# Kernel optimization log

Hardware: AMD Instinct MI355X
Metric: run time of the kernel (lower is better)

The kernel has to match this reference:

```python
import jax, jax.numpy as jnp
import numpy as np

K = 3  # knn interpolation neighbors (init kwarg k)
EPS = 1e-8


def _knn_interpolate(x, pos, pos_skip, B, k):
    # Uniform per-batch counts (guaranteed by setup_inputs) let us vectorize the
    # per-batch cdist+topk+gather chain as batched dense ops.
    Nc = pos.shape[0] // B
    Nf = pos_skip.shape[0] // B
    C = x.shape[1]
    pc = pos.reshape(B, Nc, 3)        # coarse positions
    pf = pos_skip.reshape(B, Nf, 3)   # fine (target) positions
    xc = x.reshape(B, Nc, C)          # coarse features
    # squared pairwise distances via gemm: [B, Nf, Nc]
    d2 = (jnp.sum(pf * pf, -1)[:, :, None]
          + jnp.sum(pc * pc, -1)[:, None, :]
          - 2.0 * jnp.einsum('bfd,bcd->bfc', pf, pc))
    _, idx = jax.lax.top_k(-d2, k)    # k nearest coarse indices per fine point
    b = jnp.arange(B)[:, None, None]
    nb_pos = pc[b, idx]                              # [B,Nf,k,3]
    diff = nb_pos - pf[:, :, None, :]
    dist = jnp.sqrt(jnp.sum(diff * diff, -1))        # exact same dist math as torch
    w = 1.0 / (dist + EPS)                           # [B,Nf,k]
    feats = xc[b, idx]                               # [B,Nf,k,C]
    num = jnp.einsum('bfkc,bfk->bfc', feats, w)
    den = jnp.sum(w, -1, keepdims=True) + EPS
    return (num / den).reshape(B * Nf, C)


def setup_inputs() -> dict:
    key = jax.random.key(0)
    ks = jax.random.split(key, 6)
    B, Nc, Nf, C, Cs, H = 16, 1024, 4096, 512, 256, 512
    x = jax.random.normal(ks[0], (B * Nc, C), jnp.float32)
    pos = jax.random.normal(ks[1], (B * Nc, 3), jnp.float32)
    batch = jnp.repeat(jnp.arange(B, dtype=jnp.int64), Nc)
    x_skip = jax.random.normal(ks[2], (B * Nf, Cs), jnp.float32)
    pos_skip = jax.random.normal(ks[3], (B * Nf, 3), jnp.float32)
    batch_skip = jnp.repeat(jnp.arange(B, dtype=jnp.int64), Nf)
    # MLP params (self.nn = MLP 768 -> 512 -> 512, ReLU)
    W1 = jax.random.normal(ks[4], (C + Cs, H), jnp.float32) / np.sqrt(C + Cs).astype(np.float32)
    b1 = jnp.zeros((H,), jnp.float32)
    W2 = jax.random.normal(ks[5], (H, H), jnp.float32) / np.sqrt(H).astype(np.float32)
    b2 = jnp.zeros((H,), jnp.float32)
    return dict(x=x, pos=pos, batch=batch, x_skip=x_skip, pos_skip=pos_skip,
                batch_skip=batch_skip, W1=W1, b1=b1, W2=W2, b2=b2)


def reference(x, pos, batch, x_skip, pos_skip, batch_skip, W1, b1, W2, b2):
    B = int(np.asarray(batch).max()) + 1
    h = _knn_interpolate(x, pos, pos_skip, B, K)   # [N_fine, C]
    h = jnp.concatenate([h, x_skip], axis=1)       # skip connection concat
    h = jax.nn.relu(h @ W1 + b1)
    h = jax.nn.relu(h @ W2 + b2)
    return h
```

## Files before the change

kernel.cpp:

```cpp
#include <hip/hip_runtime.h>
#include <stdint.h>

typedef __attribute__((ext_vector_type(8))) short short8;
typedef __attribute__((ext_vector_type(4))) float f32x4;

static __device__ __forceinline__ ushort f2bf(float f) {
  uint32_t u = __float_as_uint(f);
  uint32_t r = (u + 0x7FFFu + ((u >> 16) & 1u)) >> 16;
  return (ushort)r;
}
static __device__ __forceinline__ float bf2f(ushort h) {
  return __uint_as_float(((uint32_t)h) << 16);
}

static __device__ __forceinline__ void ins3b(double d, int i,
    double& b0, double& b1, double& b2, int& i0, int& i1, int& i2) {
  const bool c0 = d < b0, c1 = d < b1, c2 = d < b2;
  const double nb0 = c0 ? d : b0;
  const int    ni0 = c0 ? i : i0;
  const double nb1 = c0 ? b0 : (c1 ? d : b1);
  const int    ni1 = c0 ? i0 : (c1 ? i : i1);
  const double nb2 = c1 ? b1 : (c2 ? d : b2);
  const int    ni2 = c1 ? i1 : (c2 ? i : i2);
  b0 = nb0; b1 = nb1; b2 = nb2; i0 = ni0; i1 = ni1; i2 = ni2;
}

__global__ __launch_bounds__(256) void prep_kernel(
    const float* __restrict__ pos, const float* __restrict__ pos_skip,
    const float* __restrict__ x, const float* __restrict__ xs,
    const float* __restrict__ W1, const float* __restrict__ W2,
    int4* __restrict__ idx_out, float4* __restrict__ w_out,
    ushort* __restrict__ xbf, ushort* __restrict__ xsbf,
    ushort* __restrict__ W1at, ushort* __restrict__ W1bt,
    ushort* __restrict__ W2t)
{
  __shared__ float pc4[4096];
  if (blockIdx.x < 1024) {
    const int b   = blockIdx.x >> 6;
    const int blk = blockIdx.x & 63;
    for (int i = threadIdx.x; i < 1024; i += 256) {
      const float* ps = pos + (size_t)b * 3072 + i * 3;
      float4 v = { ps[0], ps[1], ps[2], 0.f };
      *(float4*)&pc4[i * 4] = v;
    }
    __syncthreads();

    const int p   = threadIdx.x >> 2;
    const int sub = threadIdx.x & 3;
    const int row = b * 4096 + blk * 64 + p;
    const float pxf = pos_skip[(size_t)row * 3 + 0];
    const float pyf = pos_skip[(size_t)row * 3 + 1];
    const float pzf = pos_skip[(size_t)row * 3 + 2];

    uint32_t c0 = 0xFFFFFFFFu, c1 = 0xFFFFFFFFu, c2 = 0xFFFFFFFFu, c3 = 0xFFFFFFFFu;
    auto ins4u = [&](uint32_t k) {
      const bool l0 = k < c0, l1 = k < c1, l2 = k < c2, l3 = k < c3;
      const uint32_t n0 = l0 ? k  : c0;
      const uint32_t n1 = l0 ? c0 : (l1 ? k : c1);
      const uint32_t n2 = l1 ? c1 : (l2 ? k : c2);
      const uint32_t n3 = l2 ? c2 : (l3 ? k : c3);
      c0 = n0; c1 = n1; c2 = n2; c3 = n3;
    };
#pragma unroll 4
    for (int j = 0; j < 256; ++j) {
      const int i = j * 4 + sub;
      const float4 q = *(const float4*)&pc4[i * 4];
      const float dx = q.x - pxf;
      const float dy = q.y - pyf;
      const float dz = q.z - pzf;
      const float d = fmaf(dx, dx, fmaf(dy, dy, dz * dz));
      ins4u((__float_as_uint(d) & 0xFFFFFC00u) | (uint32_t)i);
    }
#pragma unroll
    for (int m = 1; m <= 2; m <<= 1) {
      const uint32_t e0 = (uint32_t)__shfl_xor((int)c0, m);
      const uint32_t e1 = (uint32_t)__shfl_xor((int)c1, m);
      const uint32_t e2 = (uint32_t)__shfl_xor((int)c2, m);
      const uint32_t e3 = (uint32_t)__shfl_xor((int)c3, m);
      ins4u(e0); ins4u(e1); ins4u(e2); ins4u(e3);
    }
    if (sub == 0) {
      const double pxd = (double)pxf, pyd = (double)pyf, pzd = (double)pzf;
      auto exd = [&](int i) -> double {
        const double dx = (double)pc4[i * 4 + 0] - pxd;
        const double dy = (double)pc4[i * 4 + 1] - pyd;
        const double dz = (double)pc4[i * 4 + 2] - pzd;
        return dx * dx + dy * dy + dz * dz;
      };
      const int j0 = (int)(c0 & 1023u), j1 = (int)(c1 & 1023u);
      const int j2 = (int)(c2 & 1023u), j3 = (int)(c3 & 1023u);
      double b0 = 1e300, b1 = 1e300, b2 = 1e300;
      int i0 = 0, i1 = 0, i2 = 0;
      ins3b(exd(j0), j0, b0, b1, b2, i0, i1, i2);
      ins3b(exd(j1), j1, b0, b1, b2, i0, i1, i2);
      ins3b(exd(j2), j2, b0, b1, b2, i0, i1, i2);
      ins3b(exd(j3), j3, b0, b1, b2, i0, i1, i2);
      const double w0 = 1.0 / (sqrt(b0) + 1e-8);
      const double w1 = 1.0 / (sqrt(b1) + 1e-8);
      const double w2 = 1.0 / (sqrt(b2) + 1e-8);
      const double den = w0 + w1 + w2 + 1e-8;
      idx_out[row] = make_int4(i0, i1, i2, 0);
      w_out[row] = make_float4((float)(w0 / den), (float)(w1 / den), (float)(w2 / den), 0.f);
    }
  } else if (blockIdx.x < 3072) {
    const int id = (blockIdx.x - 1024) * 256 + threadIdx.x;
#pragma unroll
    for (int it = 0; it < 4; ++it) {
      const int i = id + it * 524288;
      const float4 v = *(const float4*)(x + (size_t)i * 4);
      ushort4 o = { f2bf(v.x), f2bf(v.y), f2bf(v.z), f2bf(v.w) };
      *(ushort4*)(xbf + (size_t)i * 4) = o;
    }
  } else if (blockIdx.x < 7168) {
    const int id = (blockIdx.x - 3072) * 256 + threadIdx.x;
#pragma unroll
    for (int it = 0; it < 4; ++it) {
      const int i = id + it * 1048576;
      const float4 v = *(const float4*)(xs + (size_t)i * 4);
      ushort4 o = { f2bf(v.x), f2bf(v.y), f2bf(v.z), f2bf(v.w) };
      *(ushort4*)(xsbf + (size_t)i * 4) = o;
    }
  } else {
    const int id = (blockIdx.x - 7168) * 256 + threadIdx.x;
    if (id < 262144) {
      const int n = id >> 9, k = id & 511;
      W1at[id] = f2bf(W1[(size_t)k * 512 + n]);
    } else if (id < 393216) {
      const int id2 = id - 262144;
      const int n = id2 >> 8, k = id2 & 255;
      W1bt[id2] = f2bf(W1[(size_t)(512 + k) * 512 + n]);
    } else if (id < 655360) {
      const int id3 = id - 393216;
      const int n = id3 >> 9, k = id3 & 511;
      W2t[id3] = f2bf(W2[(size_t)k * 512 + n]);
    }
  }
}

template<int K, bool OUT_BF16, bool ACT>
__global__ __launch_bounds__(512, 2) void gemm_bias_relu(
    const ushort* __restrict__ A, const ushort* __restrict__ Bt,
    const float* __restrict__ bias, void* __restrict__ Cout, int M, int N)
{
  constexpr int BM = 256, BN = 256, BK = 64, NT = K / BK;
  __shared__ ushort Asm[2][BM * BK];
  __shared__ ushort Bsm[2][BN * BK];
  const int tid  = threadIdx.x;
  const int lane = tid & 63;
  const int wave = tid >> 6;

  const int cpx  = gridDim.x >> 3;
  const int wgid = (blockIdx.x & 7) * cpx + (blockIdx.x >> 3);
  const int nbn  = N / BN;
  const int bm   = wgid / nbn;
  const int bn   = wgid - bm * nbn;
  const int row0 = bm * BM, col0 = bn * BN;
  const int wr = wave >> 2, wc = wave & 3;
  const int sbase = wave * 4096 + lane * 16;

  f32x4 acc[8][4] = {};

  auto stageA = [&](int buf, int kt) {
#pragma unroll
    for (int i = 0; i < 4; ++i) {
      const int o = sbase + i * 1024;
      const int r = o >> 7, s = (o & 127) >> 4;
      __builtin_amdgcn_global_load_lds(
          (const __attribute__((address_space(1))) void*)(A + (size_t)(row0 + r) * K + kt * BK + ((s ^ (r & 7)) << 3)),
          (__attribute__((address_space(3))) void*)((char*)&Asm[buf][0] + o), 16, 0, 0);
    }
  };
  auto stageB = [&](int buf, int kt) {
#pragma unroll
    for (int i = 0; i < 4; ++i) {
      const int o = sbase + i * 1024;
      const int r = o >> 7, s = (o & 127) >> 4;
      __builtin_amdgcn_global_load_lds(
          (const __attribute__((address_space(1))) void*)(Bt + (size_t)(col0 + r) * K + kt * BK + ((s ^ (r & 7)) << 3)),
          (__attribute__((address_space(3))) void*)((char*)&Bsm[buf][0] + o), 16, 0, 0);
    }
  };
  auto rdA = [&](int buf, int mi, int kk) -> short8 {
    const int ra = wr * 128 + mi * 16 + (lane & 15);
    const int s  = kk * 4 + (lane >> 4);
    return *(const short8*)((const char*)&Asm[buf][0] + ra * 128 + ((s ^ (ra & 7)) << 4));
  };
  auto rdB = [&](int buf, int ni, int kk) -> short8 {
    const int rb = wc * 64 + ni * 16 + (lane & 15);
    const int s  = kk * 4 + (lane >> 4);
    return *(const short8*)((const char*)&Bsm[buf][0] + rb * 128 + ((s ^ (rb & 7)) << 4));
  };

  stageA(0, 0); stageB(0, 0);
  asm volatile("s_waitcnt vmcnt(0)" ::: "memory");
  __builtin_amdgcn_s_barrier();

  int cur = 0;
#pragma unroll 1
  for (int t = 0; t < NT; ++t) {
    short8 av[4], bv[4];
#pragma unroll
    for (int mi = 0; mi < 4; ++mi) av[mi] = rdA(cur, mi, 0);
#pragma unroll
    for (int ni = 0; ni < 4; ++ni) bv[ni] = rdB(cur, ni, 0);
    if (t + 1 < NT) stageA(cur ^ 1, t + 1);
    __builtin_amdgcn_s_barrier();
    asm volatile("s_waitcnt lgkmcnt(0)" ::: "memory");
    __builtin_amdgcn_sched_barrier(0);
    __builtin_amdgcn_s_setprio(1);
#pragma unroll
    for (int mi = 0; mi < 4; ++mi)
#pragma unroll
      for (int ni = 0; ni < 4; ++ni)
        acc[mi][ni] = __builtin_amdgcn_mfma_f32_16x16x32_bf16(av[mi], bv[ni], acc[mi][ni], 0, 0, 0);
    __builtin_amdgcn_s_setprio(0);
    __builtin_amdgcn_s_barrier();
#pragma unroll
    for (int mi = 0; mi < 4; ++mi) av[mi] = rdA(cur, 4 + mi, 0);
    if (t + 1 < NT) stageB(cur ^ 1, t + 1);
    __builtin_amdgcn_s_barrier();
    asm volatile("s_waitcnt lgkmcnt(0)" ::: "memory");
    __builtin_amdgcn_sched_barrier(0);
    __builtin_amdgcn_s_setprio(1);
#pragma unroll
    for (int mi = 0; mi < 4; ++mi)
#pragma unroll
      for (int ni = 0; ni < 4; ++ni)
        acc[4 + mi][ni] = __builtin_amdgcn_mfma_f32_16x16x32_bf16(av[mi], bv[ni], acc[4 + mi][ni], 0, 0, 0);
    __builtin_amdgcn_s_setprio(0);
    __builtin_amdgcn_s_barrier();
#pragma unroll
    for (int mi = 0; mi < 4; ++mi) av[mi] = rdA(cur, mi, 1);
#pragma unroll
    for (int ni = 0; ni < 4; ++ni) bv[ni] = rdB(cur, ni, 1);
    __builtin_amdgcn_s_barrier();
    asm volatile("s_waitcnt lgkmcnt(0)" ::: "memory");
    __builtin_amdgcn_sched_barrier(0);
    __builtin_amdgcn_s_setprio(1);
#pragma unroll
    for (int mi = 0; mi < 4; ++mi)
#pragma unroll
      for (int ni = 0; ni < 4; ++ni)
        acc[mi][ni] = __builtin_amdgcn_mfma_f32_16x16x32_bf16(av[mi], bv[ni], acc[mi][ni], 0, 0, 0);
    __builtin_amdgcn_s_setprio(0);
    __builtin_amdgcn_s_barrier();
#pragma unroll
    for (int mi = 0; mi < 4; ++mi) av[mi] = rdA(cur, 4 + mi, 1);
    __builtin_amdgcn_s_barrier();
    asm volatile("s_waitcnt lgkmcnt(0)" ::: "memory");
    __builtin_amdgcn_sched_barrier(0);
    __builtin_amdgcn_s_setprio(1);
#pragma unroll
    for (int mi = 0; mi < 4; ++mi)
#pragma unroll
      for (int ni = 0; ni < 4; ++ni)
        acc[4 + mi][ni] = __builtin_amdgcn_mfma_f32_16x16x32_bf16(av[mi], bv[ni], acc[4 + mi][ni], 0, 0, 0);
    __builtin_amdgcn_s_setprio(0);
    asm volatile("s_waitcnt vmcnt(0)" ::: "memory");
    __builtin_amdgcn_s_barrier();
    cur ^= 1;
  }

  const int lc = lane & 15, lr = lane >> 4;
#pragma unroll
  for (int mi = 0; mi < 8; ++mi) {
#pragma unroll
    for (int ni = 0; ni < 4; ++ni) {
      const int col = col0 + wc * 64 + ni * 16 + lc;
      float bv2 = 0.f;
      if constexpr (ACT) bv2 = bias[col];
      const int rbase = row0 + wr * 128 + mi * 16 + lr * 4;
#pragma unroll
      for (int r = 0; r < 4; ++r) {
        float v = acc[mi][ni][r];
        if constexpr (ACT) { v += bv2; v = v > 0.f ? v : 0.f; }
        if (OUT_BF16) ((ushort*)Cout)[(size_t)(rbase + r) * N + col] = f2bf(v);
        else          ((float*)Cout)[(size_t)(rbase + r) * N + col] = v;
      }
    }
  }
}

__global__ __launch_bounds__(256, 2) void gemm128_combine(
    const ushort* __restrict__ A, const ushort* __restrict__ Bt,
    const float* __restrict__ bias, ushort* __restrict__ h2,
    const ushort* __restrict__ Ybf, const int4* __restrict__ idx3,
    const float4* __restrict__ w3)
{
  constexpr int K = 256, N = 512, BM = 128, BN = 128, BK = 64, NT = K / BK;
  __shared__ ushort Asm[2][BM * BK];
  __shared__ ushort Bsm[2][BN * BK];
  const int tid  = threadIdx.x;
  const int lane = tid & 63;
  const int wave = tid >> 6;

  const int cpx  = gridDim.x >> 3;
  const int wgid = (blockIdx.x & 7) * cpx + (blockIdx.x >> 3);
  const int nbn  = N / BN;
  const int bm   = wgid / nbn;
  const int bn   = wgid - bm * nbn;
  const int row0 = bm * BM, col0 = bn * BN;
  const int wr = wave >> 1, wc = wave & 1;
  const int so = tid * 16;

  f32x4 acc[4][4] = {};

  auto stage = [&](int buf, int kt) {
#pragma unroll
    for (int i = 0; i < 4; ++i) {
      const int o = i * 4096 + so;
      const int r = o >> 7, s = (o & 127) >> 4;
      const int cu = ((s ^ (r & 7)) << 3);
      __builtin_amdgcn_global_load_lds(
          (const __attribute__((address_space(1))) void*)(A + (size_t)(row0 + r) * K + kt * BK + cu),
          (__attribute__((address_space(3))) void*)((char*)&Asm[buf][0] + o), 16, 0, 0);
      __builtin_amdgcn_global_load_lds(
          (const __attribute__((address_space(1))) void*)(Bt + (size_t)(col0 + r) * K + kt * BK + cu),
          (__attribute__((address_space(3))) void*)((char*)&Bsm[buf][0] + o), 16, 0, 0);
    }
  };
  auto compute = [&](int buf) {
#pragma unroll
    for (int kk = 0; kk < 2; ++kk) {
      short8 af[4], bfr[4];
#pragma unroll
      for (int mi = 0; mi < 4; ++mi) {
        const int ra = wr * 64 + mi * 16 + (lane & 15);
        const int s  = kk * 4 + (lane >> 4);
        af[mi] = *(const short8*)&Asm[buf][ra * BK + ((s ^ (ra & 7)) << 3)];
      }
#pragma unroll
      for (int ni = 0; ni < 4; ++ni) {
        const int rb = wc * 64 + ni * 16 + (lane & 15);
        const int s  = kk * 4 + (lane >> 4);
        bfr[ni] = *(const short8*)&Bsm[buf][rb * BK + ((s ^ (rb & 7)) << 3)];
      }
#pragma unroll
      for (int mi = 0; mi < 4; ++mi)
#pragma unroll
        for (int ni = 0; ni < 4; ++ni)
          acc[mi][ni] = __builtin_amdgcn_mfma_f32_16x16x32_bf16(af[mi], bfr[ni], acc[mi][ni], 0, 0, 0);
    }
  };

  stage(0, 0);
  __syncthreads();
  int cur = 0;
#pragma unroll 1
  for (int kt = 0; kt < NT - 1; ++kt) {
    stage(cur ^ 1, kt + 1);
    compute(cur);
    __syncthreads();
    cur ^= 1;
  }
  compute(cur);

  const int lc = lane & 15, lr = lane >> 4;
#pragma unroll
  for (int mi = 0; mi < 4; ++mi) {
#pragma unroll
    for (int r = 0; r < 4; ++r) {
      const int row = row0 + wr * 64 + mi * 16 + lr * 4 + r;
      const int4 id = idx3[row];
      const float4 w = w3[row];
      const ushort* Yb = Ybf + (size_t)(row >> 12) * 524288;
      const ushort* y0 = Yb + (size_t)id.x * 512;
      const ushort* y1 = Yb + (size_t)id.y * 512;
      const ushort* y2 = Yb + (size_t)id.z * 512;
#pragma unroll
      for (int ni = 0; ni < 4; ++ni) {
        const int col = col0 + wc * 64 + ni * 16 + lc;
        float v = acc[mi][ni][r]
                + w.x * bf2f(y0[col])
                + w.y * bf2f(y1[col])
                + w.z * bf2f(y2[col])
                + bias[col];
        v = v > 0.f ? v : 0.f;
        h2[(size_t)row * 512 + col] = f2bf(v);
      }
    }
  }
}

extern "C" void kernel_launch(void* const* d_in, const int* in_sizes, int n_in,
                              void* d_out, int out_size, void* d_ws, size_t ws_size,
                              hipStream_t stream) {
  const float* x        = (const float*)d_in[0];
  const float* pos      = (const float*)d_in[1];
  const float* x_skip   = (const float*)d_in[3];
  const float* pos_skip = (const float*)d_in[4];
  const float* W1       = (const float*)d_in[6];
  const float* b1       = (const float*)d_in[7];
  const float* W2       = (const float*)d_in[8];
  const float* b2       = (const float*)d_in[9];

  ushort* Ybf  = (ushort*)d_out;
  ushort* xbf  = (ushort*)((char*)d_out + 83886080);
  ushort* xsbf = (ushort*)((char*)d_out + 100663296);

  char* ws = (char*)d_ws;
  ushort* h2   = (ushort*)ws;
  ushort* W1at = (ushort*)(ws + 67108864);
  ushort* W1bt = (ushort*)(ws + 67633152);
  ushort* W2t  = (ushort*)(ws + 67895296);
  int4*   idx3 = (int4*)  (ws + 68419584);
  float4* w3   = (float4*)(ws + 69468160);

  prep_kernel<<<9728, 256, 0, stream>>>(pos, pos_skip, x, x_skip, W1, W2,
                                        idx3, w3, xbf, xsbf, W1at, W1bt, W2t);
  gemm_bias_relu<512, true, false><<<128, 512, 0, stream>>>(
      xbf, W1at, nullptr, (void*)Ybf, 16384, 512);
  gemm128_combine<<<2048, 256, 0, stream>>>(xsbf, W1bt, b1, h2, Ybf, idx3, w3);
  gemm_bias_relu<512, false, true><<<512, 512, 0, stream>>>(
      h2, W2t, b2, d_out, 65536, 512);
}
```

Before: 170.0 us.

## Fuse fp32-to-bf16 activation conversion into GEMM A-tile loading

Removes the separate conversion of x and x_skip to bf16 in the prep kernel. A new 128x128 GEMM kernel instead loads fp32 A tiles into registers, converts them to bf16 and writes them to swizzled LDS. The first GEMM now uses this kernel with 512 blocks where it previously used the 256-tile kernel with 128 blocks. This avoids a full write and reread of the bf16 copies, but the GEMMs now read twice as many bytes of A and convert through registers with an explicit vmcnt wait.

```diff
diff --git a/kernel.cpp b/kernel.cpp
--- a/kernel.cpp
+++ b/kernel.cpp
@@ -27,10 +27,8 @@
 
 __global__ __launch_bounds__(256) void prep_kernel(
     const float* __restrict__ pos, const float* __restrict__ pos_skip,
-    const float* __restrict__ x, const float* __restrict__ xs,
     const float* __restrict__ W1, const float* __restrict__ W2,
     int4* __restrict__ idx_out, float4* __restrict__ w_out,
-    ushort* __restrict__ xbf, ushort* __restrict__ xsbf,
     ushort* __restrict__ W1at, ushort* __restrict__ W1bt,
     ushort* __restrict__ W2t)
 {
@@ -102,26 +100,8 @@
       idx_out[row] = make_int4(i0, i1, i2, 0);
       w_out[row] = make_float4((float)(w0 / den), (float)(w1 / den), (float)(w2 / den), 0.f);
     }
-  } else if (blockIdx.x < 3072) {
+  } else {
     const int id = (blockIdx.x - 1024) * 256 + threadIdx.x;
-#pragma unroll
-    for (int it = 0; it < 4; ++it) {
-      const int i = id + it * 524288;
-      const float4 v = *(const float4*)(x + (size_t)i * 4);
-      ushort4 o = { f2bf(v.x), f2bf(v.y), f2bf(v.z), f2bf(v.w) };
-      *(ushort4*)(xbf + (size_t)i * 4) = o;
-    }
-  } else if (blockIdx.x < 7168) {
-    const int id = (blockIdx.x - 3072) * 256 + threadIdx.x;
-#pragma unroll
-    for (int it = 0; it < 4; ++it) {
-      const int i = id + it * 1048576;
-      const float4 v = *(const float4*)(xs + (size_t)i * 4);
-      ushort4 o = { f2bf(v.x), f2bf(v.y), f2bf(v.z), f2bf(v.w) };
-      *(ushort4*)(xsbf + (size_t)i * 4) = o;
-    }
-  } else {
-    const int id = (blockIdx.x - 7168) * 256 + threadIdx.x;
     if (id < 262144) {
       const int n = id >> 9, k = id & 511;
       W1at[id] = f2bf(W1[(size_t)k * 512 + n]);
@@ -137,6 +117,145 @@
   }
 }
 
+template<int K, bool COMBINE>
+__global__ __launch_bounds__(256, 2) void gemm128_f32a(
+    const float* __restrict__ Af, const ushort* __restrict__ Bt,
+    const float* __restrict__ bias, ushort* __restrict__ Cout,
+    const ushort* __restrict__ Ybf, const int4* __restrict__ idx3,
+    const float4* __restrict__ w3)
+{
+  constexpr int N = 512, BM = 128, BN = 128, BK = 64, NT = K / BK;
+  __shared__ ushort Asm[2][BM * BK];
+  __shared__ ushort Bsm[2][BN * BK];
+  const int tid  = threadIdx.x;
+  const int lane = tid & 63;
+  const int wave = tid >> 6;
+
+  const int cpx  = gridDim.x >> 3;
+  const int wgid = (blockIdx.x & 7) * cpx + (blockIdx.x >> 3);
+  const int nbn  = N / BN;
+  const int bm   = wgid / nbn;
+  const int bn   = wgid - bm * nbn;
+  const int row0 = bm * BM, col0 = bn * BN;
+  const int wr = wave >> 1, wc = wave & 1;
+  const int so = tid * 16;
+  const int rl = tid >> 1, h = tid & 1;
+
+  f32x4 acc[4][4] = {};
+  float4 ga[8];
+
+  auto issueA = [&](int kt) {
+    const float* src = Af + (size_t)(row0 + rl) * K + kt * BK + h * 32;
+#pragma unroll
+    for (int q = 0; q < 8; ++q) ga[q] = *(const float4*)(src + q * 4);
+  };
+  auto writeA = [&](int buf) {
+    char* base = (char*)&Asm[buf][0] + rl * 128;
+#pragma unroll
+    for (int q2 = 0; q2 < 4; ++q2) {
+      const int s = h * 4 + q2;
+      short8 o;
+#pragma unroll
+      for (int e = 0; e < 4; ++e) {
+        o[e]     = (short)f2bf(((const float*)&ga[q2 * 2])[e]);
+        o[4 + e] = (short)f2bf(((const float*)&ga[q2 * 2 + 1])[e]);
+      }
+      *(short8*)(base + ((s ^ (rl & 7)) << 4)) = o;
+    }
+  };
+  auto stageB = [&](int buf, int kt) {
+#pragma unroll
+    for (int i = 0; i < 4; ++i) {
+      const int o = i * 4096 + so;
+      const int r = o >> 7, s = (o & 127) >> 4;
+      __builtin_amdgcn_global_load_lds(
+          (const __attribute__((address_space(1))) void*)(Bt + (size_t)(col0 + r) * K + kt * BK + ((s ^ (r & 7)) << 3)),
+          (__attribute__((address_space(3))) void*)((char*)&Bsm[buf][0] + o), 16, 0, 0);
+    }
+  };
+  auto compute = [&](int buf) {
+#pragma unroll
+    for (int kk = 0; kk < 2; ++kk) {
+      short8 af[4], bfr[4];
+#pragma unroll
+      for (int mi = 0; mi < 4; ++mi) {
+        const int ra = wr * 64 + mi * 16 + (lane & 15);
+        const int s  = kk * 4 + (lane >> 4);
+        af[mi] = *(const short8*)&Asm[buf][ra * BK + ((s ^ (ra & 7)) << 3)];
+      }
+#pragma unroll
+      for (int ni = 0; ni < 4; ++ni) {
+        const int rb = wc * 64 + ni * 16 + (lane & 15);
+        const int s  = kk * 4 + (lane >> 4);
+        bfr[ni] = *(const short8*)&Bsm[buf][rb * BK + ((s ^ (rb & 7)) << 3)];
+      }
+#pragma unroll
+      for (int mi = 0; mi < 4; ++mi)
+#pragma unroll
+        for (int ni = 0; ni < 4; ++ni)
+          acc[mi][ni] = __builtin_amdgcn_mfma_f32_16x16x32_bf16(af[mi], bfr[ni], acc[mi][ni], 0, 0, 0);
+    }
+  };
+
+  issueA(0); stageB(0, 0);
+  asm volatile("s_waitcnt vmcnt(0)" ::: "memory");
+  writeA(0);
+  __syncthreads();
+
+  int cur = 0;
+#pragma unroll 1
+  for (int kt = 0; kt < NT - 1; ++kt) {
+    issueA(kt + 1);
+    stageB(cur ^ 1, kt + 1);
+    compute(cur);
+    asm volatile("s_waitcnt vmcnt(0)" ::: "memory");
+    writeA(cur ^ 1);
+    __syncthreads();
+    cur ^= 1;
+  }
+  compute(cur);
+
+  const int lc = lane & 15, lr = lane >> 4;
+  if constexpr (COMBINE) {
+#pragma unroll
+    for (int mi = 0; mi < 4; ++mi) {
+#pragma unroll
+      for (int r = 0; r < 4; ++r) {
+        const int row = row0 + wr * 64 + mi * 16 + lr * 4 + r;
+        const int4 id = idx3[row];
+        const float4 w = w3[row];
+        const ushort* Yb = Ybf + (size_t)(row >> 12) * 524288;
+        const ushort* y0 = Yb + (size_t)id.x * 512;
+        const ushort* y1 = Yb + (size_t)id.y * 512;
+        const ushort* y2 = Yb + (size_t)id.z * 512;
+#pragma unroll
+        for (int ni = 0; ni < 4; ++ni) {
+          const int col = col0 + wc * 64 + ni * 16 + lc;
+          float v = acc[mi][ni][r]
+                  + w.x * bf2f(y0[col])
+                  + w.y * bf2f(y1[col])
+                  + w.z * bf2f(y2[col])
+                  + bias[col];
+          v = v > 0.f ? v : 0.f;
+          Cout[(size_t)row * 512 + col] = f2bf(v);
+        }
+      }
+    }
+  } else {
+#pragma unroll
+    for (int mi = 0; mi < 4; ++mi) {
+#pragma unroll
+      for (int ni = 0; ni < 4; ++ni) {
+        const int col = col0 + wc * 64 + ni * 16 + lc;
+        const int rbase = row0 + wr * 64 + mi * 16 + lr * 4;
+#pragma unroll
+        for (int r = 0; r < 4; ++r)
+          Cout[(size_t)(rbase + r) * N + col] = f2bf(acc[mi][ni][r]);
+      }
+    }
+  }
+}
+
 template<int K, bool OUT_BF16, bool ACT>
 __global__ __launch_bounds__(512, 2) void gemm_bias_relu(
     const ushort* __restrict__ A, const ushort* __restrict__ Bt,
@@ -281,107 +400,6 @@
   }
 }
 
-__global__ __launch_bounds__(256, 2) void gemm128_combine(
-    const ushort* __restrict__ A, const ushort* __restrict__ Bt,
-    const float* __restrict__ bias, ushort* __restrict__ h2,
-    const ushort* __restrict__ Ybf, const int4* __restrict__ idx3,
-    const float4* __restrict__ w3)
-{
-  constexpr int K = 256, N = 512, BM = 128, BN = 128, BK = 64, NT = K / BK;
-  __shared__ ushort Asm[2][BM * BK];
-  __shared__ ushort Bsm[2][BN * BK];
-  const int tid  = threadIdx.x;
-  const int lane = tid & 63;
-  const int wave = tid >> 6;
-
-  const int cpx  = gridDim.x >> 3;
-  const int wgid = (blockIdx.x & 7) * cpx + (blockIdx.x >> 3);
-  const int nbn  = N / BN;
-  const int bm   = wgid / nbn;
-  const int bn   = wgid - bm * nbn;
-  const int row0 = bm * BM, col0 = bn * BN;
-  const int wr = wave >> 1, wc = wave & 1;
-  const int so = tid * 16;
-
-  f32x4 acc[4][4] = {};
-
-  auto stage = [&](int buf, int kt) {
-#pragma unroll
-    for (int i = 0; i < 4; ++i) {
-      const int o = i * 4096 + so;
-      const int r = o >> 7, s = (o & 127) >> 4;
-      const int cu = ((s ^ (r & 7)) << 3);
-      __builtin_amdgcn_global_load_lds(
-          (const __attribute__((address_space(1))) void*)(A + (size_t)(row0 + r) * K + kt * BK + cu),
-          (__attribute__((address_space(3))) void*)((char*)&Asm[buf][0] + o), 16, 0, 0);
-      __builtin_amdgcn_global_load_lds(
-          (const __attribute__((address_space(1))) void*)(Bt + (size_t)(col0 + r) * K + kt * BK + cu),
-          (__attribute__((address_space(3))) void*)((char*)&Bsm[buf][0] + o), 16, 0, 0);
-    }
-  };
-  auto compute = [&](int buf) {
-#pragma unroll
-    for (int kk = 0; kk < 2; ++kk) {
-      short8 af[4], bfr[4];
-#pragma unroll
-      for (int mi = 0; mi < 4; ++mi) {
-        const int ra = wr * 64 + mi * 16 + (lane & 15);
-        const int s  = kk * 4 + (lane >> 4);
-        af[mi] = *(const short8*)&Asm[buf][ra * BK + ((s ^ (ra & 7)) << 3)];
-      }
-#pragma unroll
-      for (int ni = 0; ni < 4; ++ni) {
-        const int rb = wc * 64 + ni * 16 + (lane & 15);
-        const int s  = kk * 4 + (lane >> 4);
-        bfr[ni] = *(const short8*)&Bsm[buf][rb * BK + ((s ^ (rb & 7)) << 3)];
-      }
-#pragma unroll
-      for (int mi = 0; mi < 4; ++mi)
-#pragma unroll
-        for (int ni = 0; ni < 4; ++ni)
-          acc[mi][ni] = __builtin_amdgcn_mfma_f32_16x16x32_bf16(af[mi], bfr[ni], acc[mi][ni], 0, 0, 0);
-    }
-  };
-
-  stage(0, 0);
-  __syncthreads();
-  int cur = 0;
-#pragma unroll 1
-  for (int kt = 0; kt < NT - 1; ++kt) {
-    stage(cur ^ 1, kt + 1);
-    compute(cur);
-    __syncthreads();
-    cur ^= 1;
-  }
-  compute(cur);
-
-  const int lc = lane & 15, lr = lane >> 4;
-#pragma unroll
-  for (int mi = 0; mi < 4; ++mi) {
-#pragma unroll
-    for (int r = 0; r < 4; ++r) {
-      const int row = row0 + wr * 64 + mi * 16 + lr * 4 + r;
-      const int4 id = idx3[row];
-      const float4 w = w3[row];
-      const ushort* Yb = Ybf + (size_t)(row >> 12) * 524288;
-      const ushort* y0 = Yb + (size_t)id.x * 512;
-      const ushort* y1 = Yb + (size_t)id.y * 512;
-      const ushort* y2 = Yb + (size_t)id.z * 512;
-#pragma unroll
-      for (int ni = 0; ni < 4; ++ni) {
-        const int col = col0 + wc * 64 + ni * 16 + lc;
-        float v = acc[mi][ni][r]
-                + w.x * bf2f(y0[col])
-                + w.y * bf2f(y1[col])
-                + w.z * bf2f(y2[col])
-                + bias[col];
-        v = v > 0.f ? v : 0.f;
-        h2[(size_t)row * 512 + col] = f2bf(v);
-      }
-    }
-  }
-}
-
 extern "C" void kernel_launch(void* const* d_in, const int* in_sizes, int n_in,
                               void* d_out, int out_size, void* d_ws, size_t ws_size,
                               hipStream_t stream) {
@@ -395,8 +413,6 @@
   const float* b2       = (const float*)d_in[9];
 
   ushort* Ybf  = (ushort*)d_out;
-  ushort* xbf  = (ushort*)((char*)d_out + 83886080);
-  ushort* xsbf = (ushort*)((char*)d_out + 100663296);
 
   char* ws = (char*)d_ws;
   ushort* h2   = (ushort*)ws;
@@ -406,11 +422,12 @@
   int4*   idx3 = (int4*)  (ws + 68419584);
   float4* w3   = (float4*)(ws + 69468160);
 
-  prep_kernel<<<9728, 256, 0, stream>>>(pos, pos_skip, x, x_skip, W1, W2,
-                                        idx3, w3, xbf, xsbf, W1at, W1bt, W2t);
-  gemm_bias_relu<512, true, false><<<128, 512, 0, stream>>>(
-      xbf, W1at, nullptr, (void*)Ybf, 16384, 512);
-  gemm128_combine<<<2048, 256, 0, stream>>>(xsbf, W1bt, b1, h2, Ybf, idx3, w3);
+  prep_kernel<<<3584, 256, 0, stream>>>(pos, pos_skip, W1, W2,
+                                        idx3, w3, W1at, W1bt, W2t);
+  gemm128_f32a<512, false><<<512, 256, 0, stream>>>(
+      x, W1at, nullptr, Ybf, nullptr, nullptr, nullptr);
+  gemm128_f32a<256, true><<<2048, 256, 0, stream>>>(
+      x_skip, W1bt, b1, h2, Ybf, idx3, w3);
   gemm_bias_relu<512, false, true><<<512, 512, 0, stream>>>(
       h2, W2t, b2, d_out, 65536, 512);
 }
```

New measurement: 210.1 us. +23.6%, slower.
